# Performance work log

Hardware: AMD Instinct MI355X
Metric: run time of the kernel (lower is better)

## Reference

```python
import jax, jax.numpy as jnp
import numpy as np

B, S, V = 2, 2048, 50257
MIN_TOKENS_RATIO = 0.25
WARMUP_STEPS = 1000
THRESHOLD_SENSITIVITY = 0.5


def setup_inputs() -> dict:
    key = jax.random.key(0)
    k1, k2 = jax.random.split(key)
    logits = jax.random.normal(k1, (B, S, V), dtype=jnp.float32)
    targets = jax.random.randint(k2, (B, S), 0, V, dtype=jnp.int64)
    return {"logits": logits, "targets": targets, "step_count": 1000}


def _forward(logits, targets, step_count):
    vocab = logits.shape[-1]
    lf = logits.reshape(-1, vocab)          # (N, V)
    tf = targets.reshape(-1)                # (N,)
    n_tokens = lf.shape[0]

    # Single fused log-softmax pass shared by CE loss and difficulty scoring.
    logp = jax.nn.log_softmax(lf, axis=-1)  # (N, V)
    per_token_loss = -jnp.take_along_axis(logp, tf[:, None], axis=1)[:, 0]  # (N,)

    # --- difficulty scoring (no-grad in original: stop_gradient) ---
    logp_sg = jax.lax.stop_gradient(logp)
    p = jnp.exp(logp_sg)
    entropy = -jnp.sum(p * logp_sg, axis=-1)            # (N,)
    log_v = jnp.log(jnp.asarray(vocab, jnp.float32))
    ent_norm = entropy / log_v
    top2, _ = jax.lax.top_k(p, 2)                        # (N, 2)
    confidence = top2[:, 0]
    margin = top2[:, 0] - top2[:, 1]
    loss_norm = jax.lax.stop_gradient(per_token_loss) / log_v
    # 'combined' scoring: mean of normalized entropy, (1-margin), normalized loss
    difficulty = (ent_norm + (1.0 - margin) + loss_norm) / 3.0

    # --- warmup schedule + dynamic threshold ---
    progress = jnp.minimum(1.0, jnp.asarray(step_count, jnp.float32) / max(1, WARMUP_STEPS))
    base_ratio = 1.0 - progress * (1.0 - MIN_TOKENS_RATIO)
    mean_conf = jnp.mean(confidence)
    ratio = jnp.clip(base_ratio * (1.0 + THRESHOLD_SENSITIVITY * (0.5 - mean_conf)), 0.05, 1.0)

    # --- top-k selection via threshold on sorted difficulty (jit-safe dynamic k) ---
    k = jnp.clip(jnp.round(ratio * n_tokens).astype(jnp.int32), 1, n_tokens)
    sorted_desc = jnp.sort(difficulty)[::-1]
    thresh = jnp.take(sorted_desc, k - 1)
    mask = (difficulty >= thresh).astype(per_token_loss.dtype)  # (N,)

    tokens_selected = jnp.sum(mask)
    loss = jnp.sum(per_token_loss * mask) / jnp.maximum(tokens_selected, 1.0)
    return loss


def reference(logits, targets, step_count):
    return _forward(logits, targets, step_count)
```

## Files before the change

kernel.cpp:

```cpp
#include <hip/hip_runtime.h>

#define VOCAB 50257
#define NTOK 4096
#define P1_THREADS 256
#define P2_THREADS 1024
#define NEG_HUGE -3.402823466e+38f

typedef float floatx4 __attribute__((ext_vector_type(4)));

struct OS { float m, m2, Z, S1; };

__device__ __forceinline__ void os_init(OS& s) {
  s.m = NEG_HUGE; s.m2 = NEG_HUGE; s.Z = 0.0f; s.S1 = 0.0f;
}

__device__ __forceinline__ void os_merge(OS& a, float ml, float m2l, float zl, float s1l) {
  float M  = fmaxf(a.m, ml);
  float mn = fminf(a.m, ml);
  float m2 = fmaxf(fmaxf(a.m2, m2l), mn);
  float e  = __expf(mn - M);
  bool  om = a.m >= ml;
  float eo = om ? 1.0f : e;
  float en = om ? e : 1.0f;
  float S1 = eo * fmaf(a.m - M, a.Z, a.S1) + en * fmaf(ml - M, zl, s1l);
  float Z  = fmaf(eo, a.Z, en * zl);
  a.m = M; a.m2 = m2; a.Z = Z; a.S1 = S1;
}

__device__ __forceinline__ void os_update4(OS& s, floatx4 v) {
  float a  = fmaxf(v.x, v.y), b = fminf(v.x, v.y);
  float c  = fmaxf(v.z, v.w), d = fminf(v.z, v.w);
  float ml  = fmaxf(a, c);
  float m2l = fmaxf(fminf(a, c), fmaxf(b, d));
  float d0 = v.x - ml, d1 = v.y - ml, d2 = v.z - ml, d3 = v.w - ml;
  float e0 = __expf(d0), e1 = __expf(d1), e2 = __expf(d2), e3 = __expf(d3);
  float zl  = (e0 + e1) + (e2 + e3);
  float s1l = fmaf(d0, e0, fmaf(d1, e1, fmaf(d2, e2, d3 * e3)));
  os_merge(s, ml, m2l, zl, s1l);
}

__global__ __launch_bounds__(P1_THREADS) void cggr_rowstats(
    const float* __restrict__ logits, const int* __restrict__ targets,
    float* __restrict__ diff, float* __restrict__ loss, float* __restrict__ conf)
{
  const int row = blockIdx.x;
  const float* __restrict__ x = logits + (size_t)row * VOCAB;
  const int tid = threadIdx.x;

  float xt = 0.0f;
  if (tid == 0) xt = x[targets[row]];

  const int head = (4 - (row & 3)) & 3;
  const int nv4  = (VOCAB - head) >> 2;
  const floatx4* __restrict__ x4 = (const floatx4*)(x + head);

  OS s0, s1, s2, s3;
  os_init(s0); os_init(s1); os_init(s2); os_init(s3);

  int i = tid;
  for (; i + 3 * P1_THREADS < nv4; i += 4 * P1_THREADS) {
    floatx4 va = __builtin_nontemporal_load(&x4[i]);
    floatx4 vb = __builtin_nontemporal_load(&x4[i +     P1_THREADS]);
    floatx4 vc = __builtin_nontemporal_load(&x4[i + 2 * P1_THREADS]);
    floatx4 vd = __builtin_nontemporal_load(&x4[i + 3 * P1_THREADS]);
    os_update4(s0, va);
    os_update4(s1, vb);
    os_update4(s2, vc);
    os_update4(s3, vd);
  }
  for (; i < nv4; i += P1_THREADS)
    os_update4(s0, __builtin_nontemporal_load(&x4[i]));

  if (tid < head) os_merge(s1, x[tid], NEG_HUGE, 1.0f, 0.0f);
  for (int t = head + 4 * nv4 + tid; t < VOCAB; t += P1_THREADS)
    os_merge(s1, x[t], NEG_HUGE, 1.0f, 0.0f);

  os_merge(s0, s1.m, s1.m2, s1.Z, s1.S1);
  os_merge(s2, s3.m, s3.m2, s3.Z, s3.S1);
  os_merge(s0, s2.m, s2.m2, s2.Z, s2.S1);

  for (int m = 1; m < 64; m <<= 1) {
    OS o;
    o.m  = __shfl_xor(s0.m,  m);
    o.m2 = __shfl_xor(s0.m2, m);
    o.Z  = __shfl_xor(s0.Z,  m);
    o.S1 = __shfl_xor(s0.S1, m);
    os_merge(s0, o.m, o.m2, o.Z, o.S1);
  }

  __shared__ OS sred[P1_THREADS / 64];
  const int lane = tid & 63, wid = tid >> 6;
  if (lane == 0) sred[wid] = s0;
  __syncthreads();

  if (tid == 0) {
    OS a = sred[0];
    for (int w = 1; w < P1_THREADS / 64; ++w)
      os_merge(a, sred[w].m, sred[w].m2, sred[w].Z, sred[w].S1);
    float m       = a.m;
    float lnZ     = logf(a.Z);
    float ptl     = m + lnZ - xt;
    float entropy = lnZ - a.S1 / a.Z;
    float log_v   = logf((float)VOCAB);
    float cf      = 1.0f / a.Z;
    float margin  = (1.0f - __expf(a.m2 - m)) / a.Z;
    float dif     = (entropy / log_v + (1.0f - margin) + ptl / log_v) / 3.0f;
    diff[row] = dif;
    loss[row] = ptl;
    conf[row] = cf;
  }
}

__global__ __launch_bounds__(P2_THREADS) void cggr_finalize(
    const float* __restrict__ diff, const float* __restrict__ loss,
    const float* __restrict__ conf, const int* __restrict__ step_ptr,
    float* __restrict__ out)
{
  __shared__ float redF[16];
  __shared__ int   redI[2][16];
  __shared__ float redL[16], redC[16];

  const int tid = threadIdx.x, lane = tid & 63, wid = tid >> 6;

  float dv[4];
  unsigned u[4];
  float cs = 0.0f;
  #pragma unroll
  for (int j = 0; j < 4; ++j) {
    int i = tid + P2_THREADS * j;
    dv[j] = diff[i];
    cs   += conf[i];
    unsigned b = __float_as_uint(dv[j]);
    u[j] = b ^ ((b & 0x80000000u) ? 0xFFFFFFFFu : 0x80000000u);
  }

  for (int m = 1; m < 64; m <<= 1) cs += __shfl_xor(cs, m);
  if (lane == 0) redF[wid] = cs;
  __syncthreads();
  float sum = 0.0f;
  #pragma unroll
  for (int w = 0; w < 16; ++w) sum += redF[w];
  float mean_conf  = sum / (float)NTOK;
  float step       = (float)step_ptr[0];
  float progress   = fminf(1.0f, step / 1000.0f);
  float base_ratio = 1.0f - progress * (1.0f - 0.25f);
  float ratio      = base_ratio * (1.0f + 0.5f * (0.5f - mean_conf));
  ratio = fminf(fmaxf(ratio, 0.05f), 1.0f);
  int k = (int)rintf(ratio * (float)NTOK);
  k = k < 1 ? 1 : (k > NTOK ? NTOK : k);

  unsigned T = 0;
  int parity = 0;
  for (int bit = 31; bit >= 0; --bit) {
    unsigned cand = T | (1u << bit);
    int cnt = (u[0] >= cand) + (u[1] >= cand) + (u[2] >= cand) + (u[3] >= cand);
    for (int m = 1; m < 64; m <<= 1) cnt += __shfl_xor(cnt, m);
    if (lane == 0) redI[parity][wid] = cnt;
    __syncthreads();
    int tot = 0;
    #pragma unroll
    for (int w = 0; w < 16; ++w) tot += redI[parity][w];
    if (tot >= k) T = cand;
    parity ^= 1;
  }
  unsigned tb = (T & 0x80000000u) ? (T ^ 0x80000000u) : ~T;
  float thresh = __uint_as_float(tb);

  float ls = 0.0f, cn = 0.0f;
  #pragma unroll
  for (int j = 0; j < 4; ++j) {
    if (dv[j] >= thresh) { ls += loss[tid + P2_THREADS * j]; cn += 1.0f; }
  }
  for (int m = 1; m < 64; m <<= 1) {
    ls += __shfl_xor(ls, m);
    cn += __shfl_xor(cn, m);
  }
  if (lane == 0) { redL[wid] = ls; redC[wid] = cn; }
  __syncthreads();
  if (tid == 0) {
    float tl = 0.0f, tc = 0.0f;
    #pragma unroll
    for (int w = 0; w < 16; ++w) { tl += redL[w]; tc += redC[w]; }
    out[0] = tl / fmaxf(tc, 1.0f);
  }
}

extern "C" void kernel_launch(void* const* d_in, const int* in_sizes, int n_in,
                              void* d_out, int out_size, void* d_ws, size_t ws_size,
                              hipStream_t stream) {
  const float* logits  = (const float*)d_in[0];
  const int*   targets = (const int*)d_in[1];
  const int*   step    = (const int*)d_in[2];
  float* ws   = (float*)d_ws;
  float* diff = ws;
  float* loss = ws + NTOK;
  float* conf = ws + 2 * NTOK;

  hipLaunchKernelGGL(cggr_rowstats, dim3(NTOK), dim3(P1_THREADS), 0, stream,
                     logits, targets, diff, loss, conf);
  hipLaunchKernelGGL(cggr_finalize, dim3(1), dim3(P2_THREADS), 0, stream,
                     diff, loss, conf, step, (float*)d_out);
}
```

Baseline: 154.4 us.

## Fuse row stats and finalize into one kernel via last-block atomic counter

Merges the per-row statistics kernel and the single-block finalize kernel into one launch: each block bumps a global atomic counter after writing its row results, and the last block to arrive runs the threshold selection and final loss reduction with 256 threads handling 16 values each. This removes a kernel launch and its inter-kernel gap, but adds a memset launch for the counter and makes the tail reduction run on a smaller block. It also switches the logits loads from nontemporal to ordinary loads and starts the radix threshold search at bit 30, assuming positive difficulty values.

```diff
diff --git a/kernel.cpp b/kernel.cpp
--- a/kernel.cpp
+++ b/kernel.cpp
@@ -2,8 +2,7 @@
 
 #define VOCAB 50257
 #define NTOK 4096
-#define P1_THREADS 256
-#define P2_THREADS 1024
+#define THREADS 256
 #define NEG_HUGE -3.402823466e+38f
 
 typedef float floatx4 __attribute__((ext_vector_type(4)));
@@ -39,13 +38,22 @@
   os_merge(s, ml, m2l, zl, s1l);
 }
 
-__global__ __launch_bounds__(P1_THREADS) void cggr_rowstats(
+__global__ __launch_bounds__(THREADS) void cggr_fused(
     const float* __restrict__ logits, const int* __restrict__ targets,
-    float* __restrict__ diff, float* __restrict__ loss, float* __restrict__ conf)
+    const int* __restrict__ step_ptr,
+    float* __restrict__ diff, float* __restrict__ loss, float* __restrict__ conf,
+    int* __restrict__ counter, float* __restrict__ out)
 {
   const int row = blockIdx.x;
   const float* __restrict__ x = logits + (size_t)row * VOCAB;
-  const int tid = threadIdx.x;
+  const int tid  = threadIdx.x;
+  const int lane = tid & 63, wid = tid >> 6;
+
+  __shared__ OS sred[THREADS / 64];
+  __shared__ int winner_s;
+  __shared__ float redF[THREADS / 64];
+  __shared__ int   redI[2][THREADS / 64];
+  __shared__ float redL[THREADS / 64], redC[THREADS / 64];
 
   float xt = 0.0f;
   if (tid == 0) xt = x[targets[row]];
@@ -58,21 +66,20 @@
   os_init(s0); os_init(s1); os_init(s2); os_init(s3);
 
   int i = tid;
-  for (; i + 3 * P1_THREADS < nv4; i += 4 * P1_THREADS) {
-    floatx4 va = __builtin_nontemporal_load(&x4[i]);
-    floatx4 vb = __builtin_nontemporal_load(&x4[i +     P1_THREADS]);
-    floatx4 vc = __builtin_nontemporal_load(&x4[i + 2 * P1_THREADS]);
-    floatx4 vd = __builtin_nontemporal_load(&x4[i + 3 * P1_THREADS]);
+  for (; i + 3 * THREADS < nv4; i += 4 * THREADS) {
+    floatx4 va = x4[i];
+    floatx4 vb = x4[i +     THREADS];
+    floatx4 vc = x4[i + 2 * THREADS];
+    floatx4 vd = x4[i + 3 * THREADS];
     os_update4(s0, va);
     os_update4(s1, vb);
     os_update4(s2, vc);
     os_update4(s3, vd);
   }
-  for (; i < nv4; i += P1_THREADS)
-    os_update4(s0, __builtin_nontemporal_load(&x4[i]));
+  for (; i < nv4; i += THREADS) os_update4(s0, x4[i]);
 
   if (tid < head) os_merge(s1, x[tid], NEG_HUGE, 1.0f, 0.0f);
-  for (int t = head + 4 * nv4 + tid; t < VOCAB; t += P1_THREADS)
+  for (int t = head + 4 * nv4 + tid; t < VOCAB; t += THREADS)
     os_merge(s1, x[t], NEG_HUGE, 1.0f, 0.0f);
 
   os_merge(s0, s1.m, s1.m2, s1.Z, s1.S1);
@@ -88,14 +95,12 @@
     os_merge(s0, o.m, o.m2, o.Z, o.S1);
   }
 
-  __shared__ OS sred[P1_THREADS / 64];
-  const int lane = tid & 63, wid = tid >> 6;
   if (lane == 0) sred[wid] = s0;
   __syncthreads();
 
   if (tid == 0) {
     OS a = sred[0];
-    for (int w = 1; w < P1_THREADS / 64; ++w)
+    for (int w = 1; w < THREADS / 64; ++w)
       os_merge(a, sred[w].m, sred[w].m2, sred[w].Z, sred[w].S1);
     float m       = a.m;
     float lnZ     = logf(a.Z);
@@ -108,29 +113,22 @@
     diff[row] = dif;
     loss[row] = ptl;
     conf[row] = cf;
-  }
-}
-
-__global__ __launch_bounds__(P2_THREADS) void cggr_finalize(
-    const float* __restrict__ diff, const float* __restrict__ loss,
-    const float* __restrict__ conf, const int* __restrict__ step_ptr,
-    float* __restrict__ out)
-{
-  __shared__ float redF[16];
-  __shared__ int   redI[2][16];
-  __shared__ float redL[16], redC[16];
-
-  const int tid = threadIdx.x, lane = tid & 63, wid = tid >> 6;
-
-  float dv[4];
-  unsigned u[4];
+    __threadfence();
+    int old = atomicAdd(counter, 1);
+    winner_s = (old == (int)gridDim.x - 1) ? 1 : 0;
+  }
+  __syncthreads();
+  if (!winner_s) return;
+  __threadfence();
+
+  unsigned u[16];
   float cs = 0.0f;
   #pragma unroll
-  for (int j = 0; j < 4; ++j) {
-    int i = tid + P2_THREADS * j;
-    dv[j] = diff[i];
-    cs   += conf[i];
-    unsigned b = __float_as_uint(dv[j]);
+  for (int j = 0; j < 16; ++j) {
+    int idx = tid + THREADS * j;
+    float d = diff[idx];
+    cs += conf[idx];
+    unsigned b = __float_as_uint(d);
     u[j] = b ^ ((b & 0x80000000u) ? 0xFFFFFFFFu : 0x80000000u);
   }
 
@@ -139,7 +137,7 @@
   __syncthreads();
   float sum = 0.0f;
   #pragma unroll
-  for (int w = 0; w < 16; ++w) sum += redF[w];
+  for (int w = 0; w < THREADS / 64; ++w) sum += redF[w];
   float mean_conf  = sum / (float)NTOK;
   float step       = (float)step_ptr[0];
   float progress   = fminf(1.0f, step / 1000.0f);
@@ -149,27 +147,27 @@
   int k = (int)rintf(ratio * (float)NTOK);
   k = k < 1 ? 1 : (k > NTOK ? NTOK : k);
 
-  unsigned T = 0;
+  unsigned T = 0x80000000u;
   int parity = 0;
-  for (int bit = 31; bit >= 0; --bit) {
+  for (int bit = 30; bit >= 0; --bit) {
     unsigned cand = T | (1u << bit);
-    int cnt = (u[0] >= cand) + (u[1] >= cand) + (u[2] >= cand) + (u[3] >= cand);
+    int cnt = 0;
+    #pragma unroll
+    for (int j = 0; j < 16; ++j) cnt += (u[j] >= cand);
     for (int m = 1; m < 64; m <<= 1) cnt += __shfl_xor(cnt, m);
     if (lane == 0) redI[parity][wid] = cnt;
     __syncthreads();
     int tot = 0;
     #pragma unroll
-    for (int w = 0; w < 16; ++w) tot += redI[parity][w];
+    for (int w = 0; w < THREADS / 64; ++w) tot += redI[parity][w];
     if (tot >= k) T = cand;
     parity ^= 1;
   }
-  unsigned tb = (T & 0x80000000u) ? (T ^ 0x80000000u) : ~T;
-  float thresh = __uint_as_float(tb);
 
   float ls = 0.0f, cn = 0.0f;
   #pragma unroll
-  for (int j = 0; j < 4; ++j) {
-    if (dv[j] >= thresh) { ls += loss[tid + P2_THREADS * j]; cn += 1.0f; }
+  for (int j = 0; j < 16; ++j) {
+    if (u[j] >= T) { ls += loss[tid + THREADS * j]; cn += 1.0f; }
   }
   for (int m = 1; m < 64; m <<= 1) {
     ls += __shfl_xor(ls, m);
@@ -180,7 +178,7 @@
   if (tid == 0) {
     float tl = 0.0f, tc = 0.0f;
     #pragma unroll
-    for (int w = 0; w < 16; ++w) { tl += redL[w]; tc += redC[w]; }
+    for (int w = 0; w < THREADS / 64; ++w) { tl += redL[w]; tc += redC[w]; }
     out[0] = tl / fmaxf(tc, 1.0f);
   }
 }
@@ -195,9 +193,10 @@
   float* diff = ws;
   float* loss = ws + NTOK;
   float* conf = ws + 2 * NTOK;
-
-  hipLaunchKernelGGL(cggr_rowstats, dim3(NTOK), dim3(P1_THREADS), 0, stream,
-                     logits, targets, diff, loss, conf);
-  hipLaunchKernelGGL(cggr_finalize, dim3(1), dim3(P2_THREADS), 0, stream,
-                     diff, loss, conf, step, (float*)d_out);
-}
+  int*   counter = (int*)(ws + 3 * NTOK);
+
+  hipMemsetAsync((void*)counter, 0, sizeof(int), stream);
+
+  hipLaunchKernelGGL(cggr_fused, dim3(NTOK), dim3(THREADS), 0, stream,
+                     logits, targets, step, diff, loss, conf, counter, (float*)d_out);
+}
```

Result: slower. 367.6 us (+138.0%).
